# Kernel optimization log

Measured on AMD Instinct MI355X. Metric: run time of the kernel, lower is better.

The kernel has to match this reference:

```python
import jax, jax.numpy as jnp
import numpy as np

H = 512; W = 512; PH = 16; PW = 16; Q = 3; JITTER = 1e-06
NH = H // PH; NW = W // PW; P = NH * NW
B = 64


def setup_inputs() -> dict:
    key = jax.random.key(0)
    k0, k1, k2, k3, k4 = jax.random.split(key, 5)
    x = jax.random.normal(k0, (B, H, W), dtype=jnp.float32)
    logits = jax.random.normal(k1, (P, Q), dtype=jnp.float32)
    mu = jax.random.normal(k2, (P, Q, 2), dtype=jnp.float32) * 0.3
    sigma = jnp.exp(jax.random.normal(k3, (P, Q, 2), dtype=jnp.float32) * 0.3)
    bias = jax.random.normal(k4, (P, PH, PW), dtype=jnp.float32)
    return {"x": x, "logits": logits, "mu": mu, "sigma": sigma, "bias": bias}


def _make_S(logits, mu, sigma):
    # logits: (P,Q), mu/sigma: (P,Q,2) -> S: (P,PH,PW)
    w = jax.nn.softmax(logits, axis=-1)            # (P,Q)
    fy = jnp.fft.fftfreq(PH).astype(jnp.float32)   # (PH,)
    fx = jnp.fft.fftfreq(PW).astype(jnp.float32)   # (PW,)
    mu_y = mu[..., 0][:, :, None, None]            # (P,Q,1,1)
    mu_x = mu[..., 1][:, :, None, None]
    sg_y = sigma[..., 0][:, :, None, None]
    sg_x = sigma[..., 1][:, :, None, None]
    fy_b = fy[None, None, :, None]                 # (1,1,PH,1)
    fx_b = fx[None, None, None, :]                 # (1,1,1,PW)
    g1 = jnp.exp(-0.5 * (((fy_b - mu_y) / sg_y) ** 2 + ((fx_b - mu_x) / sg_x) ** 2))
    g2 = jnp.exp(-0.5 * (((fy_b + mu_y) / sg_y) ** 2 + ((fx_b + mu_x) / sg_x) ** 2))
    # weighted sum over mixture components Q
    S = jnp.einsum('pq,pqhw->phw', w, g1 + g2) + JITTER
    return S


def reference(x, logits, mu, sigma, bias):
    # x: (B,H,W) -> (B,H,W)
    S = _make_S(logits, mu, sigma)                                  # (P,PH,PW)
    x_p = x.reshape(B, NH, PH, NW, PW)
    x_p = x_p.transpose(1, 3, 0, 2, 4).reshape(P, B, PH, PW)        # (P,B,PH,PW)
    Xf = jnp.fft.fftn(x_p, axes=(-2, -1))                           # complex64
    y_p = jnp.fft.ifftn(Xf * S[:, None, :, :], axes=(-2, -1)).real  # (P,B,PH,PW)
    y_p = y_p + bias[:, None, :, :]
    y = y_p.reshape(NH, NW, B, PH, PW)
    y = y.transpose(2, 0, 3, 1, 4).reshape(B, H, W)
    return y
```

## Files before the change

kernel.cpp:

```cpp
#include <hip/hip_runtime.h>
#include <math.h>

#define HH 512
#define WW 512
#define PHH 16
#define PWW 16
#define QQ 3
#define NHH 32
#define NWW 32
#define PP 1024
#define BB 64

__device__ __forceinline__ void wfence() {
  asm volatile("" ::: "memory");
}

template <int SGN, int T>
__device__ __forceinline__ void bfly(float& ar, float& ai, float& br, float& bi) {
  float tr, ti;
  if constexpr (T == 0) {
    tr = br;
    ti = bi;
  } else if constexpr (T == 4) {
    if constexpr (SGN > 0) { tr = bi;  ti = -br; }
    else                   { tr = -bi; ti = br;  }
  } else if constexpr (T == 2) {
    constexpr float c = 0.70710678118654752440f;
    if constexpr (SGN > 0) { tr = c * (br + bi); ti = c * (bi - br); }
    else                   { tr = c * (br - bi); ti = c * (bi + br); }
  } else if constexpr (T == 6) {
    constexpr float c = 0.70710678118654752440f;
    if constexpr (SGN > 0) { tr = c * (bi - br);  ti = -c * (br + bi); }
    else                   { tr = -c * (br + bi); ti = c * (br - bi);  }
  } else {
    constexpr float c1 = 0.92387953251128675613f;
    constexpr float s1 = 0.38268343236508977173f;
    constexpr float wr = (T == 1) ? c1 : (T == 3) ? s1 : (T == 5) ? -s1 : -c1;
    constexpr float wi0 = (T == 1) ? -s1 : (T == 3) ? -c1 : (T == 5) ? -c1 : -s1;
    constexpr float wi = (SGN > 0) ? wi0 : -wi0;
    tr = br * wr - bi * wi;
    ti = br * wi + bi * wr;
  }
  br = ar - tr;
  bi = ai - ti;
  ar = ar + tr;
  ai = ai + ti;
}

template <int SGN>
__device__ __forceinline__ void fft16(float re[16], float im[16]) {
#define SW_(a, b)                              \
  { float t = re[a]; re[a] = re[b]; re[b] = t; \
    t = im[a]; im[a] = im[b]; im[b] = t; }
  SW_(1, 8) SW_(2, 4) SW_(3, 12) SW_(5, 10) SW_(7, 14) SW_(11, 13)
#undef SW_
#define BF_(a, b, T) bfly<SGN, T>(re[a], im[a], re[b], im[b]);
  BF_(0, 1, 0) BF_(2, 3, 0) BF_(4, 5, 0) BF_(6, 7, 0)
  BF_(8, 9, 0) BF_(10, 11, 0) BF_(12, 13, 0) BF_(14, 15, 0)
  BF_(0, 2, 0) BF_(1, 3, 4) BF_(4, 6, 0) BF_(5, 7, 4)
  BF_(8, 10, 0) BF_(9, 11, 4) BF_(12, 14, 0) BF_(13, 15, 4)
  BF_(0, 4, 0) BF_(1, 5, 2) BF_(2, 6, 4) BF_(3, 7, 6)
  BF_(8, 12, 0) BF_(9, 13, 2) BF_(10, 14, 4) BF_(11, 15, 6)
  BF_(0, 8, 0) BF_(1, 9, 1) BF_(2, 10, 2) BF_(3, 11, 3)
  BF_(4, 12, 4) BF_(5, 13, 5) BF_(6, 14, 6) BF_(7, 15, 7)
#undef BF_
}

__global__ __launch_bounds__(256)
__attribute__((amdgpu_waves_per_eu(1, 4)))
void psm_kernel(
    const float* __restrict__ x, const float* __restrict__ logits,
    const float* __restrict__ mu, const float* __restrict__ sigma,
    const float* __restrict__ bias, float* __restrict__ out) {
  __shared__ float S_lds[256];
  __shared__ float tbuf[16 * 272];

  const int tid = threadIdx.x;
  const int p = blockIdx.x >> 2;
  const int b0 = (blockIdx.x & 3) << 4;
  const int g = tid >> 4;
  const int r = tid & 15;
  const int b = b0 + g;
  const int nh = p >> 5;
  const int nw = p & 31;

  const size_t rowoff =
      (size_t)b * (HH * WW) + (size_t)(nh * PHH + r) * WW + (size_t)(nw * PWW);
  const float* xrow = x + rowoff;
  float re[16], im[16];
#pragma unroll
  for (int c4 = 0; c4 < 4; ++c4) {
    const float4 v = ((const float4*)xrow)[c4];
    re[c4 * 4 + 0] = v.x;
    re[c4 * 4 + 1] = v.y;
    re[c4 * 4 + 2] = v.z;
    re[c4 * 4 + 3] = v.w;
  }

  {
    const int fy_i = tid >> 4;
    const int fx_i = tid & 15;
    const float fy = (float)(fy_i < 8 ? fy_i : fy_i - 16) * (1.0f / 16.0f);
    const float fx = (float)(fx_i < 8 ? fx_i : fx_i - 16) * (1.0f / 16.0f);
    const float l0 = logits[p * QQ + 0];
    const float l1 = logits[p * QQ + 1];
    const float l2 = logits[p * QQ + 2];
    const float lm = fmaxf(l0, fmaxf(l1, l2));
    const float e0 = __expf(l0 - lm);
    const float e1 = __expf(l1 - lm);
    const float e2 = __expf(l2 - lm);
    const float inv = 1.0f / (e0 + e1 + e2);
    const float wq[3] = {e0 * inv, e1 * inv, e2 * inv};
    float s = 0.0f;
#pragma unroll
    for (int q = 0; q < QQ; ++q) {
      const float muy = mu[(p * QQ + q) * 2 + 0];
      const float mux = mu[(p * QQ + q) * 2 + 1];
      const float isy = 1.0f / sigma[(p * QQ + q) * 2 + 0];
      const float isx = 1.0f / sigma[(p * QQ + q) * 2 + 1];
      const float dy1 = (fy - muy) * isy;
      const float dx1 = (fx - mux) * isx;
      const float dy2 = (fy + muy) * isy;
      const float dx2 = (fx + mux) * isx;
      const float g1 = __expf(-0.5f * (dy1 * dy1 + dx1 * dx1));
      const float g2 = __expf(-0.5f * (dy2 * dy2 + dx2 * dx2));
      s += wq[q] * (g1 + g2);
    }
    S_lds[tid] = (s + 1e-6f) * (1.0f / 256.0f);
  }
  __syncthreads();

#pragma unroll
  for (int c = 0; c < 16; ++c) im[c] = 0.0f;

  fft16<1>(re, im);

  float* m = &tbuf[g * 272];
#pragma unroll
  for (int c = 0; c < 16; ++c) m[r * 17 + c] = re[c];
  wfence();
#pragma unroll
  for (int k = 0; k < 16; ++k) re[k] = m[k * 17 + r];
  wfence();
#pragma unroll
  for (int c = 0; c < 16; ++c) m[r * 17 + c] = im[c];
  wfence();
#pragma unroll
  for (int k = 0; k < 16; ++k) im[k] = m[k * 17 + r];
  wfence();

  fft16<1>(re, im);
#pragma unroll
  for (int k = 0; k < 16; ++k) {
    const float s = S_lds[k * 16 + r];
    re[k] *= s;
    im[k] *= s;
  }
  fft16<-1>(re, im);

#pragma unroll
  for (int k = 0; k < 16; ++k) m[k * 17 + r] = re[k];
  wfence();
#pragma unroll
  for (int c = 0; c < 16; ++c) re[c] = m[r * 17 + c];
  wfence();
#pragma unroll
  for (int k = 0; k < 16; ++k) m[k * 17 + r] = im[k];
  wfence();
#pragma unroll
  for (int c = 0; c < 16; ++c) im[c] = m[r * 17 + c];

  fft16<-1>(re, im);

  const float* brow = bias + (size_t)p * 256 + (size_t)r * 16;
  float* orow = out + rowoff;
#pragma unroll
  for (int c4 = 0; c4 < 4; ++c4) {
    const float4 bv = ((const float4*)brow)[c4];
    float4 o;
    o.x = re[c4 * 4 + 0] + bv.x;
    o.y = re[c4 * 4 + 1] + bv.y;
    o.z = re[c4 * 4 + 2] + bv.z;
    o.w = re[c4 * 4 + 3] + bv.w;
    ((float4*)orow)[c4] = o;
  }
}

extern "C" void kernel_launch(void* const* d_in, const int* in_sizes, int n_in,
                              void* d_out, int out_size, void* d_ws,
                              size_t ws_size, hipStream_t stream) {
  (void)in_sizes;
  (void)n_in;
  (void)out_size;
  (void)d_ws;
  (void)ws_size;
  const float* x = (const float*)d_in[0];
  const float* logits = (const float*)d_in[1];
  const float* mu = (const float*)d_in[2];
  const float* sigma = (const float*)d_in[3];
  const float* bias = (const float*)d_in[4];
  float* out = (float*)d_out;

  psm_kernel<<<dim3(PP * 4), dim3(256), 0, stream>>>(x, logits, mu, sigma,
                                                     bias, out);
}
```

Measured before the change: 146.7 us.

## Process four batch groups per block with register prefetch of next tile

```diff
diff --git a/kernel.cpp b/kernel.cpp
--- a/kernel.cpp
+++ b/kernel.cpp
@@ -67,7 +67,7 @@
 }
 
 __global__ __launch_bounds__(256)
-__attribute__((amdgpu_waves_per_eu(1, 4)))
+__attribute__((amdgpu_waves_per_eu(1, 3)))
 void psm_kernel(
     const float* __restrict__ x, const float* __restrict__ logits,
     const float* __restrict__ mu, const float* __restrict__ sigma,
@@ -76,25 +76,26 @@
   __shared__ float tbuf[16 * 272];
 
   const int tid = threadIdx.x;
-  const int p = blockIdx.x >> 2;
-  const int b0 = (blockIdx.x & 3) << 4;
+  const int p = blockIdx.x;
   const int g = tid >> 4;
   const int r = tid & 15;
-  const int b = b0 + g;
   const int nh = p >> 5;
   const int nw = p & 31;
 
-  const size_t rowoff =
-      (size_t)b * (HH * WW) + (size_t)(nh * PHH + r) * WW + (size_t)(nw * PWW);
-  const float* xrow = x + rowoff;
+  const size_t rowbase =
+      (size_t)(nh * PHH + r) * WW + (size_t)(nw * PWW);
+
   float re[16], im[16];
-#pragma unroll
-  for (int c4 = 0; c4 < 4; ++c4) {
-    const float4 v = ((const float4*)xrow)[c4];
-    re[c4 * 4 + 0] = v.x;
-    re[c4 * 4 + 1] = v.y;
-    re[c4 * 4 + 2] = v.z;
-    re[c4 * 4 + 3] = v.w;
+  {
+    const float* xrow = x + (size_t)g * (HH * WW) + rowbase;
+#pragma unroll
+    for (int c4 = 0; c4 < 4; ++c4) {
+      const float4 v = ((const float4*)xrow)[c4];
+      re[c4 * 4 + 0] = v.x;
+      re[c4 * 4 + 1] = v.y;
+      re[c4 * 4 + 2] = v.z;
+      re[c4 * 4 + 3] = v.w;
+    }
   }
 
   {
@@ -130,59 +131,83 @@
   }
   __syncthreads();
 
-#pragma unroll
-  for (int c = 0; c < 16; ++c) im[c] = 0.0f;
-
-  fft16<1>(re, im);
-
   float* m = &tbuf[g * 272];
-#pragma unroll
-  for (int c = 0; c < 16; ++c) m[r * 17 + c] = re[c];
-  wfence();
-#pragma unroll
-  for (int k = 0; k < 16; ++k) re[k] = m[k * 17 + r];
-  wfence();
-#pragma unroll
-  for (int c = 0; c < 16; ++c) m[r * 17 + c] = im[c];
-  wfence();
-#pragma unroll
-  for (int k = 0; k < 16; ++k) im[k] = m[k * 17 + r];
-  wfence();
-
-  fft16<1>(re, im);
-#pragma unroll
-  for (int k = 0; k < 16; ++k) {
-    const float s = S_lds[k * 16 + r];
-    re[k] *= s;
-    im[k] *= s;
-  }
-  fft16<-1>(re, im);
-
-#pragma unroll
-  for (int k = 0; k < 16; ++k) m[k * 17 + r] = re[k];
-  wfence();
-#pragma unroll
-  for (int c = 0; c < 16; ++c) re[c] = m[r * 17 + c];
-  wfence();
-#pragma unroll
-  for (int k = 0; k < 16; ++k) m[k * 17 + r] = im[k];
-  wfence();
-#pragma unroll
-  for (int c = 0; c < 16; ++c) im[c] = m[r * 17 + c];
-
-  fft16<-1>(re, im);
-
   const float* brow = bias + (size_t)p * 256 + (size_t)r * 16;
-  float* orow = out + rowoff;
-#pragma unroll
-  for (int c4 = 0; c4 < 4; ++c4) {
-    const float4 bv = ((const float4*)brow)[c4];
-    float4 o;
-    o.x = re[c4 * 4 + 0] + bv.x;
-    o.y = re[c4 * 4 + 1] + bv.y;
-    o.z = re[c4 * 4 + 2] + bv.z;
-    o.w = re[c4 * 4 + 3] + bv.w;
-    ((float4*)orow)[c4] = o;
+
+#pragma unroll
+  for (int i = 0; i < 4; ++i) {
+    wfence();
+
+    float nre[16];
+    if (i < 3) {
+      const float* xnext =
+          x + (size_t)(16 * (i + 1) + g) * (HH * WW) + rowbase;
+#pragma unroll
+      for (int c4 = 0; c4 < 4; ++c4) {
+        const float4 v = ((const float4*)xnext)[c4];
+        nre[c4 * 4 + 0] = v.x;
+        nre[c4 * 4 + 1] = v.y;
+        nre[c4 * 4 + 2] = v.z;
+        nre[c4 * 4 + 3] = v.w;
+      }
+    }
+
+#pragma unroll
+    for (int c = 0; c < 16; ++c) im[c] = 0.0f;
+    fft16<1>(re, im);
+
+#pragma unroll
+    for (int c = 0; c < 16; ++c) m[r * 17 + c] = re[c];
+    wfence();
+#pragma unroll
+    for (int k = 0; k < 16; ++k) re[k] = m[k * 17 + r];
+    wfence();
+#pragma unroll
+    for (int c = 0; c < 16; ++c) m[r * 17 + c] = im[c];
+    wfence();
+#pragma unroll
+    for (int k = 0; k < 16; ++k) im[k] = m[k * 17 + r];
+    wfence();
+
+    fft16<1>(re, im);
+#pragma unroll
+    for (int k = 0; k < 16; ++k) {
+      const float s = S_lds[k * 16 + r];
+      re[k] *= s;
+      im[k] *= s;
+    }
+    fft16<-1>(re, im);
+
+#pragma unroll
+    for (int k = 0; k < 16; ++k) m[k * 17 + r] = re[k];
+    wfence();
+#pragma unroll
+    for (int c = 0; c < 16; ++c) re[c] = m[r * 17 + c];
+    wfence();
+#pragma unroll
+    for (int k = 0; k < 16; ++k) m[k * 17 + r] = im[k];
+    wfence();
+#pragma unroll
+    for (int c = 0; c < 16; ++c) im[c] = m[r * 17 + c];
+
+    fft16<-1>(re, im);
+
+    float* orow = out + (size_t)(16 * i + g) * (HH * WW) + rowbase;
+#pragma unroll
+    for (int c4 = 0; c4 < 4; ++c4) {
+      const float4 bv = ((const float4*)brow)[c4];
+      float4 o;
+      o.x = re[c4 * 4 + 0] + bv.x;
+      o.y = re[c4 * 4 + 1] + bv.y;
+      o.z = re[c4 * 4 + 2] + bv.z;
+      o.w = re[c4 * 4 + 3] + bv.w;
+      ((float4*)orow)[c4] = o;
+    }
+
+    if (i < 3) {
+#pragma unroll
+      for (int c = 0; c < 16; ++c) re[c] = nre[c];
+    }
   }
 }
 
@@ -201,6 +226,6 @@
   const float* bias = (const float*)d_in[4];
   float* out = (float*)d_out;
 
-  psm_kernel<<<dim3(PP * 4), dim3(256), 0, stream>>>(x, logits, mu, sigma,
-                                                     bias, out);
-}
+  psm_kernel<<<dim3(PP), dim3(256), 0, stream>>>(x, logits, mu, sigma,
+                                                 bias, out);
+}
```

Result: slower. 157.3 us (+7.3%).

## Pack two real batch images into one complex FFT per thread

Applied to the files above, without the earlier changes.

```diff
diff --git a/kernel.cpp b/kernel.cpp
--- a/kernel.cpp
+++ b/kernel.cpp
@@ -67,7 +67,7 @@
 }
 
 __global__ __launch_bounds__(256)
-__attribute__((amdgpu_waves_per_eu(1, 4)))
+__attribute__((amdgpu_waves_per_eu(1, 3)))
 void psm_kernel(
     const float* __restrict__ x, const float* __restrict__ logits,
     const float* __restrict__ mu, const float* __restrict__ sigma,
@@ -76,25 +76,38 @@
   __shared__ float tbuf[16 * 272];
 
   const int tid = threadIdx.x;
-  const int p = blockIdx.x >> 2;
-  const int b0 = (blockIdx.x & 3) << 4;
+  const int p = blockIdx.x >> 1;
+  const int chunk = blockIdx.x & 1;
   const int g = tid >> 4;
   const int r = tid & 15;
-  const int b = b0 + g;
   const int nh = p >> 5;
   const int nw = p & 31;
 
-  const size_t rowoff =
-      (size_t)b * (HH * WW) + (size_t)(nh * PHH + r) * WW + (size_t)(nw * PWW);
-  const float* xrow = x + rowoff;
+  const int b_re = chunk * 32 + 2 * g;
+
+  const size_t rowbase = (size_t)(nh * PHH + r) * WW + (size_t)(nw * PWW);
+  const size_t off_re = (size_t)b_re * (HH * WW) + rowbase;
+
   float re[16], im[16];
-#pragma unroll
-  for (int c4 = 0; c4 < 4; ++c4) {
-    const float4 v = ((const float4*)xrow)[c4];
-    re[c4 * 4 + 0] = v.x;
-    re[c4 * 4 + 1] = v.y;
-    re[c4 * 4 + 2] = v.z;
-    re[c4 * 4 + 3] = v.w;
+  {
+    const float* xa = x + off_re;
+    const float* xb = xa + (size_t)(HH * WW);
+#pragma unroll
+    for (int c4 = 0; c4 < 4; ++c4) {
+      const float4 va = ((const float4*)xa)[c4];
+      re[c4 * 4 + 0] = va.x;
+      re[c4 * 4 + 1] = va.y;
+      re[c4 * 4 + 2] = va.z;
+      re[c4 * 4 + 3] = va.w;
+    }
+#pragma unroll
+    for (int c4 = 0; c4 < 4; ++c4) {
+      const float4 vb = ((const float4*)xb)[c4];
+      im[c4 * 4 + 0] = vb.x;
+      im[c4 * 4 + 1] = vb.y;
+      im[c4 * 4 + 2] = vb.z;
+      im[c4 * 4 + 3] = vb.w;
+    }
   }
 
   {
@@ -130,9 +143,6 @@
   }
   __syncthreads();
 
-#pragma unroll
-  for (int c = 0; c < 16; ++c) im[c] = 0.0f;
-
   fft16<1>(re, im);
 
   float* m = &tbuf[g * 272];
@@ -173,16 +183,22 @@
   fft16<-1>(re, im);
 
   const float* brow = bias + (size_t)p * 256 + (size_t)r * 16;
-  float* orow = out + rowoff;
+  float* oa = out + off_re;
+  float* ob = oa + (size_t)(HH * WW);
 #pragma unroll
   for (int c4 = 0; c4 < 4; ++c4) {
     const float4 bv = ((const float4*)brow)[c4];
-    float4 o;
-    o.x = re[c4 * 4 + 0] + bv.x;
-    o.y = re[c4 * 4 + 1] + bv.y;
-    o.z = re[c4 * 4 + 2] + bv.z;
-    o.w = re[c4 * 4 + 3] + bv.w;
-    ((float4*)orow)[c4] = o;
+    float4 o1, o2;
+    o1.x = re[c4 * 4 + 0] + bv.x;
+    o1.y = re[c4 * 4 + 1] + bv.y;
+    o1.z = re[c4 * 4 + 2] + bv.z;
+    o1.w = re[c4 * 4 + 3] + bv.w;
+    o2.x = im[c4 * 4 + 0] + bv.x;
+    o2.y = im[c4 * 4 + 1] + bv.y;
+    o2.z = im[c4 * 4 + 2] + bv.z;
+    o2.w = im[c4 * 4 + 3] + bv.w;
+    ((float4*)oa)[c4] = o1;
+    ((float4*)ob)[c4] = o2;
   }
 }
 
@@ -201,6 +217,6 @@
   const float* bias = (const float*)d_in[4];
   float* out = (float*)d_out;
 
-  psm_kernel<<<dim3(PP * 4), dim3(256), 0, stream>>>(x, logits, mu, sigma,
+  psm_kernel<<<dim3(PP * 2), dim3(256), 0, stream>>>(x, logits, mu, sigma,
                                                      bias, out);
 }
```

Result: slower. 153.1 us (+4.4%).
